# Optimization experiments

Measured on AMD Instinct MI355X. Metric: run time of the kernel, lower is better.

Reference implementation:

```python
import jax, jax.numpy as jnp
import numpy as np

N = 50000      # nodes
E = 600000     # edges (avg degree 12)
C = 128        # in/out channels
NF = 256       # SchNet num_filters (hardcoded in module)
EC = 64        # edge_channels (RBF expansion)


def ssp(x):
    # shifted softplus used by SchNet
    return jax.nn.softplus(x) - jnp.log(2.0).astype(x.dtype)


def setup_inputs() -> dict:
    key = jax.random.key(0)
    ks = jax.random.split(key, 16)
    def w(k, shape, fan_in):
        return jax.random.normal(k, shape, jnp.float32) * (1.0 / np.sqrt(fan_in))
    return {
        "x": jax.random.normal(ks[0], (N, C), jnp.float32),
        "edge_index": jax.random.randint(ks[1], (2, E), 0, N, jnp.int32),
        "edge_attr": jax.random.normal(ks[2], (E, EC), jnp.float32),
        "x_pos": jax.random.normal(ks[3], (N, 3), jnp.float32),
        # SchNet filter network: Linear(EC,NF) -> ssp -> Linear(NF,NF)
        "W_f1": w(ks[4], (EC, NF), EC), "b_f1": jnp.zeros((NF,), jnp.float32),
        "W_f2": w(ks[5], (NF, NF), NF), "b_f2": jnp.zeros((NF,), jnp.float32),
        # CFConv lin1 (no bias), lin2, then output lin3
        "W_lin1": w(ks[6], (C, NF), C),
        "W_lin2": w(ks[7], (NF, C), NF), "b_lin2": jnp.zeros((C,), jnp.float32),
        "W_lin3": w(ks[8], (C, C), C), "b_lin3": jnp.zeros((C,), jnp.float32),
        # edge MLP: Linear(EC + C, C) -> Tanh
        "W_e": w(ks[9], (EC + C, C), EC + C), "b_e": jnp.zeros((C,), jnp.float32),
    }


def reference(x, edge_index, edge_attr, x_pos,
              W_f1, b_f1, W_f2, b_f2,
              W_lin1, W_lin2, b_lin2, W_lin3, b_lin3,
              W_e, b_e):
    n = x.shape[0]
    row, col = edge_index[0], edge_index[1]

    # SchNet interaction (cfconv): edge filter net on edge_attr
    Wf = ssp(edge_attr @ W_f1 + b_f1) @ W_f2 + b_f2      # [E, NF]
    h = x @ W_lin1                                        # [N, NF]
    msg = h[col] * Wf                                     # [E, NF] gather + modulate
    agg = jax.ops.segment_sum(msg, row, num_segments=n)   # [N, NF] scatter-sum
    y = ssp(agg @ W_lin2 + b_lin2) @ W_lin3 + b_lin3      # [N, C]

    # relu + residual skip
    x_out = jax.nn.relu(y) + x

    # edge gather-MLP with residual on edge_attr
    e_in = jnp.concatenate([edge_attr, x_out[row] + x_out[col]], axis=-1)  # [E, EC+C]
    e_out = jnp.tanh(e_in @ W_e + b_e) + edge_attr if False else jnp.tanh(e_in @ W_e + b_e)
    # note: original adds residual only on edge_attr channels; shapes differ (C vs EC)
    # Linear maps to in_channels=C... but residual is `+ edge_attr` [E,EC]. In the repo
    # edge_channels == in_channels is required for this add; here EC != C, so we
    # follow the module math with EC projected: use the faithful form below.
    return x_out, e_out
```

## Files before the change

### kernel.cpp

```cpp
#include <hip/hip_runtime.h>

#define NN  50000
#define NE  600000
#define CC  128
#define NFF 256
#define ECH 64
#define EIN 192

typedef __attribute__((ext_vector_type(8))) short bf16x8;
typedef __attribute__((ext_vector_type(4))) short bf16x4;
typedef __attribute__((ext_vector_type(4))) float f32x4;
typedef __attribute__((ext_vector_type(4))) unsigned u32x4;
typedef __attribute__((ext_vector_type(2))) unsigned u32x2;

__device__ __forceinline__ float sspf(float v) {
    float e = __expf(-fabsf(v));
    return fmaxf(v, 0.f) + __logf(1.f + e) - 0.693147180559945f;
}
__device__ __forceinline__ float ftanh(float v) {
    float e = __expf(-2.f * fabsf(v));
    float r = (1.f - e) / (1.f + e);
    return copysignf(r, v);
}
__device__ __forceinline__ short bf16r(float f) {
    unsigned u = __float_as_uint(f);
    u = (u + 0x7FFFu + ((u >> 16) & 1u)) >> 16;
    return (short)u;
}
__device__ __forceinline__ unsigned cvtpk(float lo, float hi) {
    unsigned r;
    asm("v_cvt_pk_bf16_f32 %0, %1, %2" : "=v"(r) : "v"(lo), "v"(hi));
    return r;
}
__device__ __forceinline__ float bfu_lo(unsigned u) { return __uint_as_float(u << 16); }
__device__ __forceinline__ float bfu_hi(unsigned u) { return __uint_as_float(u & 0xffff0000u); }

#define PO_WF1 0
#define PO_WF2 16384
#define PO_WE  81920
#define PO_WL1 106496
#define PO_WL2 139264
#define PO_WL3 172032
#define P_TOT  188416
__global__ void kpack(const float* __restrict__ Wf1, const float* __restrict__ Wf2,
                      const float* __restrict__ We,  const float* __restrict__ Wl1,
                      const float* __restrict__ Wl2, const float* __restrict__ Wl3,
                      short* __restrict__ p) {
    int i = blockIdx.x * 256 + threadIdx.x;
    if (i < PO_WF2) {
        int t = i - PO_WF1;
        int j = t & 7, lane = (t >> 3) & 63, n16 = (t >> 9) & 15, ks = t >> 13;
        p[i] = bf16r(Wf1[(ks * 32 + (lane >> 4) * 8 + j) * NFF + n16 * 16 + (lane & 15)]);
    } else if (i < PO_WE) {
        int t = i - PO_WF2;
        int j = t & 7, lane = (t >> 3) & 63, n16 = (t >> 9) & 15, ks = t >> 13;
        int kp = ks * 32 + (lane >> 4) * 8 + j;
        int k = (kp >> 6) * 64 + (kp & 3) * 16 + ((kp >> 2) & 15);
        p[i] = bf16r(Wf2[k * NFF + n16 * 16 + (lane & 15)]);
    } else if (i < PO_WL1) {
        int t = i - PO_WE;
        int j = t & 7, lane = (t >> 3) & 63, n16 = (t >> 9) & 7, ks = t >> 12;
        p[i] = bf16r(We[(ks * 32 + (lane >> 4) * 8 + j) * CC + n16 * 16 + (lane & 15)]);
    } else if (i < PO_WL2) {
        int t = i - PO_WL1;
        int j = t & 7, lane = (t >> 3) & 63, n16 = (t >> 9) & 15, ks = t >> 13;
        p[i] = bf16r(Wl1[(ks * 32 + (lane >> 4) * 8 + j) * NFF + n16 * 16 + (lane & 15)]);
    } else if (i < PO_WL3) {
        int t = i - PO_WL2;
        int j = t & 7, lane = (t >> 3) & 63, n16 = (t >> 9) & 7, ks = t >> 12;
        int kp = ks * 32 + (lane >> 4) * 8 + j;
        int k = (kp >> 6) * 64 + (kp & 3) * 16 + ((kp >> 2) & 15);
        p[i] = bf16r(Wl2[k * CC + n16 * 16 + (lane & 15)]);
    } else if (i < P_TOT) {
        int t = i - PO_WL3;
        int j = t & 7, lane = (t >> 3) & 63, n16 = (t >> 9) & 7, ks = t >> 12;
        int kp = ks * 32 + (lane >> 4) * 8 + j;
        int k = (kp >> 5) * 32 + (kp & 1) * 16 + ((kp & 31) >> 1);
        p[i] = bf16r(Wl3[k * CC + n16 * 16 + (lane & 15)]);
    }
}

__global__ void k0_zero(float* __restrict__ p, long n4) {
    long i = (long)blockIdx.x * blockDim.x + threadIdx.x;
    long stride = (long)gridDim.x * blockDim.x;
    float4 z = {0.f, 0.f, 0.f, 0.f};
    for (; i < n4; i += stride) ((float4*)p)[i] = z;
}

__global__ void k_cnt(const int* __restrict__ eidx, int* __restrict__ cnt) {
    int e = blockIdx.x * 256 + threadIdx.x;
    if (e < NE) atomicAdd(&cnt[eidx[e]], 1);
}

__global__ __launch_bounds__(256) void k_scan1(const int* __restrict__ cnt,
                                               int* __restrict__ offw,
                                               int* __restrict__ bsum) {
    __shared__ int sw_[4];
    int i = blockIdx.x * 256 + threadIdx.x;
    int lane = threadIdx.x & 63, wv = threadIdx.x >> 6;
    int v = (i < NN) ? cnt[i] : 0;
    int inc = v;
    #pragma unroll
    for (int d = 1; d < 64; d <<= 1) {
        int t = __shfl_up(inc, d, 64);
        if (lane >= d) inc += t;
    }
    if (lane == 63) sw_[wv] = inc;
    __syncthreads();
    int woff = 0;
    #pragma unroll
    for (int k = 0; k < 4; ++k) woff += (k < wv) ? sw_[k] : 0;
    if (i < NN) offw[i] = woff + inc - v;
    if (threadIdx.x == 255) bsum[blockIdx.x] = woff + inc;
}

__global__ __launch_bounds__(256) void k_scan2(int* __restrict__ bsum, int nb) {
    __shared__ int sw_[4];
    int t = threadIdx.x;
    int lane = t & 63, wv = t >> 6;
    int v = (t < nb) ? bsum[t] : 0;
    int inc = v;
    #pragma unroll
    for (int d = 1; d < 64; d <<= 1) {
        int s = __shfl_up(inc, d, 64);
        if (lane >= d) inc += s;
    }
    if (lane == 63) sw_[wv] = inc;
    __syncthreads();
    int woff = 0;
    #pragma unroll
    for (int k = 0; k < 4; ++k) woff += (k < wv) ? sw_[k] : 0;
    if (t < nb) bsum[t] = woff + inc - v;
}

__global__ void k_scan3(int* __restrict__ offw, const int* __restrict__ bsum,
                        int* __restrict__ rowptr) {
    int i = blockIdx.x * 256 + threadIdx.x;
    if (i < NN) {
        int v = offw[i] + bsum[blockIdx.x];
        offw[i] = v;
        rowptr[i] = v;
    }
    if (i == 0) rowptr[NN] = NE;
}

__global__ void k_scatter(const int* __restrict__ eidx, int* __restrict__ offw,
                          int* __restrict__ dest) {
    int e = blockIdx.x * 256 + threadIdx.x;
    if (e < NE) dest[e] = atomicAdd(&offw[eidx[e]], 1);
}

__global__ __launch_bounds__(256) void k1_h(const float* __restrict__ x,
                                            const short* __restrict__ pW,
                                            short* __restrict__ h) {
    __shared__ char xS[32 * 256];
    int n0 = blockIdx.x * 32;
    int tid = threadIdx.x;
    int lane = tid & 63, w = tid >> 6, q = lane >> 4, l15 = lane & 15;
    {
        int r = tid >> 3, seg = tid & 7;
        int rr = min(n0 + r, NN - 1);
        const float4* src = (const float4*)(x + (size_t)rr * CC + seg * 16);
        float4 f0 = src[0], f1 = src[1], f2 = src[2], f3 = src[3];
        u32x4 c0 = {cvtpk(f0.x, f0.y), cvtpk(f0.z, f0.w), cvtpk(f1.x, f1.y), cvtpk(f1.z, f1.w)};
        u32x4 c1 = {cvtpk(f2.x, f2.y), cvtpk(f2.z, f2.w), cvtpk(f3.x, f3.y), cvtpk(f3.z, f3.w)};
        int sw = (r & 7) << 4;
        *(u32x4*)(xS + r * 256 + ((seg * 32) ^ sw)) = c0;
        *(u32x4*)(xS + r * 256 + ((seg * 32 + 16) ^ sw)) = c1;
    }
    __syncthreads();

    f32x4 acc[2][4];
    #pragma unroll
    for (int mf = 0; mf < 2; ++mf)
        #pragma unroll
        for (int nf = 0; nf < 4; ++nf) acc[mf][nf] = f32x4{0.f, 0.f, 0.f, 0.f};

    #pragma unroll
    for (int ks = 0; ks < 4; ++ks) {
        bf16x8 a[2];
        #pragma unroll
        for (int mf = 0; mf < 2; ++mf) {
            int row = mf * 16 + l15;
            a[mf] = *(const bf16x8*)(xS + row * 256 + ((ks * 64 + q * 16) ^ ((row & 7) << 4)));
        }
        #pragma unroll
        for (int nf = 0; nf < 4; ++nf) {
            bf16x8 b = *(const bf16x8*)(pW + PO_WL1 + (((ks * 16 + w * 4 + nf) * 64) + lane) * 8);
            #pragma unroll
            for (int mf = 0; mf < 2; ++mf)
                acc[mf][nf] = __builtin_amdgcn_mfma_f32_16x16x32_bf16(a[mf], b, acc[mf][nf], 0, 0, 0);
        }
    }
    #pragma unroll
    for (int mf = 0; mf < 2; ++mf) {
        #pragma unroll
        for (int r = 0; r < 4; ++r) {
            int n = n0 + mf * 16 + q * 4 + r;
            if (n < NN) {
                u32x2 v = {cvtpk(acc[mf][0][r], acc[mf][1][r]),
                           cvtpk(acc[mf][2][r], acc[mf][3][r])};
                *(u32x2*)(h + (size_t)n * NFF + w * 64 + l15 * 4) = v;
            }
        }
    }
}

__global__ __launch_bounds__(256, 4) void k2a_msg(
        const float* __restrict__ ea, const int* __restrict__ eidx,
        const int* __restrict__ dest,
        const short* __restrict__ pW, const float* __restrict__ bf1v,
        const float* __restrict__ bf2v,
        const short* __restrict__ h, short* __restrict__ msg) {
    __shared__ char t1S[64 * 512];
    __shared__ int colS[64], destS[64];
    char* eaS = t1S;
    int e0 = blockIdx.x * 64;
    int tid = threadIdx.x;
    int lane = tid & 63, w = tid >> 6;
    int q = lane >> 4, l15 = lane & 15;

    if (tid < 64) {
        colS[tid] = eidx[NE + e0 + tid];
        destS[tid] = dest[e0 + tid];
    }

    {
        int r = tid >> 2, cp = tid & 3;
        const float4* src = (const float4*)(ea + (size_t)(e0 + r) * ECH + cp * 16);
        float4 f0 = src[0], f1 = src[1], f2 = src[2], f3 = src[3];
        u32x4 c0 = {cvtpk(f0.x, f0.y), cvtpk(f0.z, f0.w), cvtpk(f1.x, f1.y), cvtpk(f1.z, f1.w)};
        u32x4 c1 = {cvtpk(f2.x, f2.y), cvtpk(f2.z, f2.w), cvtpk(f3.x, f3.y), cvtpk(f3.z, f3.w)};
        int sw = (r & 7) << 4;
        *(u32x4*)(eaS + r * 128 + ((cp * 32) ^ sw)) = c0;
        *(u32x4*)(eaS + r * 128 + ((cp * 32 + 16) ^ sw)) = c1;
    }
    __syncthreads();

    f32x4 acc[4][4];
    #pragma unroll
    for (int mf = 0; mf < 4; ++mf)
        #pragma unroll
        for (int nf = 0; nf < 4; ++nf) acc[mf][nf] = f32x4{0.f, 0.f, 0.f, 0.f};

    #pragma unroll
    for (int ks = 0; ks < 2; ++ks) {
        bf16x8 a[4];
        #pragma unroll
        for (int mf = 0; mf < 4; ++mf) {
            int row = mf * 16 + l15;
            a[mf] = *(const bf16x8*)(eaS + row * 128 + ((ks * 64 + q * 16) ^ ((row & 7) << 4)));
        }
        #pragma unroll
        for (int nf = 0; nf < 4; ++nf) {
            bf16x8 b = *(const bf16x8*)(pW + PO_WF1 + (((ks * 16 + w * 4 + nf) * 64) + lane) * 8);
            #pragma unroll
            for (int mf = 0; mf < 4; ++mf)
                acc[mf][nf] = __builtin_amdgcn_mfma_f32_16x16x32_bf16(a[mf], b, acc[mf][nf], 0, 0, 0);
        }
    }
    __syncthreads();

    {
        float bia[4];
        #pragma unroll
        for (int nf = 0; nf < 4; ++nf) bia[nf] = bf1v[w * 64 + nf * 16 + l15];
        #pragma unroll
        for (int mf = 0; mf < 4; ++mf) {
            #pragma unroll
            for (int r = 0; r < 4; ++r) {
                int row = mf * 16 + q * 4 + r;
                u32x2 v = {cvtpk(sspf(acc[mf][0][r] + bia[0]), sspf(acc[mf][1][r] + bia[1])),
                           cvtpk(sspf(acc[mf][2][r] + bia[2]), sspf(acc[mf][3][r] + bia[3]))};
                *(u32x2*)(t1S + row * 512 + ((w * 128 + l15 * 8) ^ ((row & 7) << 4))) = v;
            }
        }
    }
    __syncthreads();

    #pragma unroll
    for (int mf = 0; mf < 4; ++mf)
        #pragma unroll
        for (int nf = 0; nf < 4; ++nf) acc[mf][nf] = f32x4{0.f, 0.f, 0.f, 0.f};

    for (int ks = 0; ks < 8; ++ks) {
        bf16x8 a[4];
        #pragma unroll
        for (int mf = 0; mf < 4; ++mf) {
            int row = mf * 16 + l15;
            a[mf] = *(const bf16x8*)(t1S + row * 512 + ((ks * 64 + q * 16) ^ ((row & 7) << 4)));
        }
        #pragma unroll
        for (int nf = 0; nf < 4; ++nf) {
            bf16x8 b = *(const bf16x8*)(pW + PO_WF2 + (((ks * 16 + w * 4 + nf) * 64) + lane) * 8);
            #pragma unroll
            for (int mf = 0; mf < 4; ++mf)
                acc[mf][nf] = __builtin_amdgcn_mfma_f32_16x16x32_bf16(a[mf], b, acc[mf][nf], 0, 0, 0);
        }
    }
    __syncthreads();

    {
        int r = tid >> 2, ch = tid & 3;
        const short* hp = h + (size_t)colS[r] * NFF;
        int sw = (r & 7) << 4;
        #pragma unroll
        for (int i = 0; i < 8; ++i) {
            int chunk = ch + i * 4;
            bf16x8 v = *(const bf16x8*)(hp + chunk * 8);
            *(bf16x8*)(t1S + r * 512 + ((chunk * 16) ^ sw)) = v;
        }
    }
    __syncthreads();

    {
        float bia[4];
        #pragma unroll
        for (int nf = 0; nf < 4; ++nf) bia[nf] = bf2v[w * 64 + nf * 16 + l15];
        #pragma unroll
        for (int mf = 0; mf < 4; ++mf) {
            #pragma unroll
            for (int r = 0; r < 4; ++r) {
                int eloc = mf * 16 + q * 4 + r;
                u32x2 hv = *(const u32x2*)(t1S + eloc * 512 + ((w * 128 + l15 * 8) ^ ((eloc & 7) << 4)));
                float m0 = bfu_lo(hv[0]) * (acc[mf][0][r] + bia[0]);
                float m1 = bfu_hi(hv[0]) * (acc[mf][1][r] + bia[1]);
                float m2 = bfu_lo(hv[1]) * (acc[mf][2][r] + bia[2]);
                float m3 = bfu_hi(hv[1]) * (acc[mf][3][r] + bia[3]);
                u32x2 out = {cvtpk(m0, m1), cvtpk(m2, m3)};
                *(u32x2*)(msg + (size_t)destS[eloc] * NFF + w * 64 + l15 * 4) = out;
            }
        }
    }
}

__global__ __launch_bounds__(256) void k3_node(
        const short* __restrict__ msg, const int* __restrict__ rowptr,
        const short* __restrict__ pW, const float* __restrict__ bl2,
        const float* __restrict__ bl3,
        const float* __restrict__ x, float* __restrict__ xo) {
    __shared__ char aggS[32 * 512];
    __shared__ char t2S[32 * 256];
    int n0 = blockIdx.x * 32;
    int tid = threadIdx.x;
    int lane = tid & 63, w = tid >> 6, q = lane >> 4, l15 = lane & 15;

    {
        int nd = tid >> 3, c0 = (tid & 7) * 32;
        int n = n0 + nd;
        int p0 = 0, p1 = 0;
        if (n < NN) { p0 = rowptr[n]; p1 = rowptr[n + 1]; }
        float a[32];
        #pragma unroll
        for (int i = 0; i < 32; ++i) a[i] = 0.f;
        for (int p = p0; p < p1; ++p) {
            const short* mrow = msg + (size_t)p * NFF + c0;
            #pragma unroll
            for (int j = 0; j < 4; ++j) {
                u32x4 v = *(const u32x4*)(mrow + j * 8);
                #pragma unroll
                for (int k = 0; k < 4; ++k) {
                    a[j * 8 + 2 * k]     += bfu_lo(v[k]);
                    a[j * 8 + 2 * k + 1] += bfu_hi(v[k]);
                }
            }
        }
        int sw = (nd & 7) << 4;
        #pragma unroll
        for (int j = 0; j < 4; ++j) {
            u32x4 v = {cvtpk(a[j * 8 + 0], a[j * 8 + 1]), cvtpk(a[j * 8 + 2], a[j * 8 + 3]),
                       cvtpk(a[j * 8 + 4], a[j * 8 + 5]), cvtpk(a[j * 8 + 6], a[j * 8 + 7])};
            *(u32x4*)(aggS + nd * 512 + (((c0 + j * 8) * 2) ^ sw)) = v;
        }
    }
    __syncthreads();

    f32x4 acc[2][2];
    #pragma unroll
    for (int mf = 0; mf < 2; ++mf)
        #pragma unroll
        for (int nf = 0; nf < 2; ++nf) acc[mf][nf] = f32x4{0.f, 0.f, 0.f, 0.f};
    for (int ks = 0; ks < 8; ++ks) {
        bf16x8 a[2];
        #pragma unroll
        for (int mf = 0; mf < 2; ++mf) {
            int row = mf * 16 + l15;
            a[mf] = *(const bf16x8*)(aggS + row * 512 + ((ks * 64 + q * 16) ^ ((row & 7) << 4)));
        }
        #pragma unroll
        for (int nf = 0; nf < 2; ++nf) {
            bf16x8 b = *(const bf16x8*)(pW + PO_WL2 + (((ks * 8 + w * 2 + nf) * 64) + lane) * 8);
            #pragma unroll
            for (int mf = 0; mf < 2; ++mf)
                acc[mf][nf] = __builtin_amdgcn_mfma_f32_16x16x32_bf16(a[mf], b, acc[mf][nf], 0, 0, 0);
        }
    }
    {
        float bia[2];
        #pragma unroll
        for (int nf = 0; nf < 2; ++nf) bia[nf] = bl2[w * 32 + nf * 16 + l15];
        #pragma unroll
        for (int mf = 0; mf < 2; ++mf) {
            #pragma unroll
            for (int r = 0; r < 4; ++r) {
                int row = mf * 16 + q * 4 + r;
                unsigned u = cvtpk(sspf(acc[mf][0][r] + bia[0]), sspf(acc[mf][1][r] + bia[1]));
                *(unsigned*)(t2S + row * 256 + ((w * 64 + l15 * 4) ^ ((row & 7) << 4))) = u;
            }
        }
    }
    __syncthreads();

    f32x4 acc2[2][2];
    #pragma unroll
    for (int mf = 0; mf < 2; ++mf)
        #pragma unroll
        for (int nf = 0; nf < 2; ++nf) acc2[mf][nf] = f32x4{0.f, 0.f, 0.f, 0.f};
    #pragma unroll
    for (int ks = 0; ks < 4; ++ks) {
        bf16x8 a[2];
        #pragma unroll
        for (int mf = 0; mf < 2; ++mf) {
            int row = mf * 16 + l15;
            a[mf] = *(const bf16x8*)(t2S + row * 256 + ((ks * 64 + q * 16) ^ ((row & 7) << 4)));
        }
        #pragma unroll
        for (int nf = 0; nf < 2; ++nf) {
            bf16x8 b = *(const bf16x8*)(pW + PO_WL3 + (((ks * 8 + w * 2 + nf) * 64) + lane) * 8);
            #pragma unroll
            for (int mf = 0; mf < 2; ++mf)
                acc2[mf][nf] = __builtin_amdgcn_mfma_f32_16x16x32_bf16(a[mf], b, acc2[mf][nf], 0, 0, 0);
        }
    }
    #pragma unroll
    for (int nf = 0; nf < 2; ++nf) {
        int col = w * 32 + nf * 16 + l15;
        float bias = bl3[col];
        #pragma unroll
        for (int mf = 0; mf < 2; ++mf) {
            #pragma unroll
            for (int r = 0; r < 4; ++r) {
                int n = n0 + mf * 16 + q * 4 + r;
                if (n < NN) {
                    size_t o = (size_t)n * CC + col;
                    xo[o] = fmaxf(acc2[mf][nf][r] + bias, 0.f) + x[o];
                }
            }
        }
    }
}

__global__ __launch_bounds__(256) void k4_mfma(
        const float* __restrict__ ea, const int* __restrict__ eidx,
        const float* __restrict__ xo, const short* __restrict__ pW,
        const float* __restrict__ bev, float* __restrict__ eo) {
    __shared__ char aS[64 * 384];
    int e0 = blockIdx.x * 64;
    int tid = threadIdx.x;
    int lane = tid & 63, w = tid >> 6;
    int q = lane >> 4, l15 = lane & 15;

    {
        int r = tid >> 2, cp = tid & 3;
        const float4* src = (const float4*)(ea + (size_t)(e0 + r) * ECH + cp * 16);
        float4 f0 = src[0], f1 = src[1], f2 = src[2], f3 = src[3];
        u32x4 c0 = {cvtpk(f0.x, f0.y), cvtpk(f0.z, f0.w), cvtpk(f1.x, f1.y), cvtpk(f1.z, f1.w)};
        u32x4 c1 = {cvtpk(f2.x, f2.y), cvtpk(f2.z, f2.w), cvtpk(f3.x, f3.y), cvtpk(f3.z, f3.w)};
        int sw = (r & 7) << 4;
        *(u32x4*)(aS + r * 384 + ((cp * 32) ^ sw)) = c0;
        *(u32x4*)(aS + r * 384 + ((cp * 32 + 16) ^ sw)) = c1;
    }
    {
        int e = tid >> 2, p = tid & 3;
        int rr = eidx[e0 + e], cc = eidx[NE + e0 + e];
        const float4* xr = (const float4*)(xo + (size_t)rr * CC);
        const float4* xc = (const float4*)(xo + (size_t)cc * CC);
        int sw = (e & 7) << 4;
        #pragma unroll
        for (int it = 0; it < 8; ++it) {
            int fi = p + it * 4;
            float4 va = xr[fi], vb = xc[fi];
            u32x2 hv = {cvtpk(va.x + vb.x, va.y + vb.y), cvtpk(va.z + vb.z, va.w + vb.w)};
            int byte = (ECH + fi * 4) * 2;
            *(u32x2*)(aS + e * 384 + (byte ^ sw)) = hv;
        }
    }
    __syncthreads();

    f32x4 acc[8];
    #pragma unroll
    for (int nf = 0; nf < 8; ++nf) acc[nf] = f32x4{0.f, 0.f, 0.f, 0.f};

    #pragma unroll
    for (int ks = 0; ks < 6; ++ks) {
        int row = w * 16 + l15;
        bf16x8 a = *(const bf16x8*)(aS + row * 384 + ((ks * 64 + q * 16) ^ ((row & 7) << 4)));
        #pragma unroll
        for (int nf = 0; nf < 8; ++nf) {
            bf16x8 b = *(const bf16x8*)(pW + PO_WE + (((ks * 8 + nf) * 64) + lane) * 8);
            acc[nf] = __builtin_amdgcn_mfma_f32_16x16x32_bf16(a, b, acc[nf], 0, 0, 0);
        }
    }
    #pragma unroll
    for (int nf = 0; nf < 8; ++nf) {
        int col = nf * 16 + l15;
        float bias = bev[col];
        #pragma unroll
        for (int r = 0; r < 4; ++r) {
            int e = e0 + w * 16 + q * 4 + r;
            eo[(size_t)e * CC + col] = ftanh(acc[nf][r] + bias);
        }
    }
}

extern "C" void kernel_launch(void* const* d_in, const int* in_sizes, int n_in,
                              void* d_out, int out_size, void* d_ws, size_t ws_size,
                              hipStream_t stream) {
    const float* x   = (const float*)d_in[0];
    const int*   ei  = (const int*)d_in[1];
    const float* ea  = (const float*)d_in[2];
    const float* Wf1 = (const float*)d_in[4];
    const float* bf1 = (const float*)d_in[5];
    const float* Wf2 = (const float*)d_in[6];
    const float* bf2 = (const float*)d_in[7];
    const float* Wl1 = (const float*)d_in[8];
    const float* Wl2 = (const float*)d_in[9];
    const float* bl2 = (const float*)d_in[10];
    const float* Wl3 = (const float*)d_in[11];
    const float* bl3 = (const float*)d_in[12];
    const float* We  = (const float*)d_in[13];
    const float* be  = (const float*)d_in[14];

    float* xo = (float*)d_out;
    float* eo = xo + (size_t)NN * CC;

    short* h   = (short*)xo;
    short* msg = (short*)eo;

    short* pW    = (short*)d_ws;
    int* dest    = (int*)((char*)d_ws + 393216);
    int* cnt     = dest + NE;
    int* offw    = cnt + NN;
    int* rowptr  = offw + NN;
    int* bsum    = rowptr + NN + 1;

    const int NB = (NN + 255) / 256;

    kpack<<<P_TOT / 256, 256, 0, stream>>>(Wf1, Wf2, We, Wl1, Wl2, Wl3, pW);
    k0_zero<<<49, 256, 0, stream>>>((float*)cnt, NN / 4);
    k_cnt<<<(NE + 255) / 256, 256, 0, stream>>>(ei, cnt);
    k_scan1<<<NB, 256, 0, stream>>>(cnt, offw, bsum);
    k_scan2<<<1, 256, 0, stream>>>(bsum, NB);
    k_scan3<<<NB, 256, 0, stream>>>(offw, bsum, rowptr);
    k_scatter<<<(NE + 255) / 256, 256, 0, stream>>>(ei, offw, dest);
    k1_h<<<(NN + 31) / 32, 256, 0, stream>>>(x, pW, h);
    k2a_msg<<<NE / 64, 256, 0, stream>>>(ea, ei, dest, pW, bf1, bf2, h, msg);
    k3_node<<<(NN + 31) / 32, 256, 0, stream>>>(msg, rowptr, pW, bl2, bl3, x, xo);
    k4_mfma<<<NE / 64, 256, 0, stream>>>(ea, ei, xo, pW, be, eo);
}
```

Measured before the change: 548.1 us.

## Presort edges by row and fuse segment-sum into message kernel

```diff
diff --git a/kernel.cpp b/kernel.cpp
--- a/kernel.cpp
+++ b/kernel.cpp
@@ -144,10 +144,25 @@
     if (i == 0) rowptr[NN] = NE;
 }
 
-__global__ void k_scatter(const int* __restrict__ eidx, int* __restrict__ offw,
-                          int* __restrict__ dest) {
+__global__ void k_scatter(const int* __restrict__ eidx, const float* __restrict__ ea,
+                          int* __restrict__ offw, short* __restrict__ ea_s,
+                          int* __restrict__ col_s, int* __restrict__ row_s) {
     int e = blockIdx.x * 256 + threadIdx.x;
-    if (e < NE) dest[e] = atomicAdd(&offw[eidx[e]], 1);
+    if (e >= NE) return;
+    int r = eidx[e], c = eidx[NE + e];
+    int pos = atomicAdd(&offw[r], 1);
+    col_s[pos] = c;
+    row_s[pos] = r;
+    const float4* src = (const float4*)(ea + (size_t)e * ECH);
+    short* dst = ea_s + (size_t)pos * ECH;
+    #pragma unroll
+    for (int i = 0; i < 4; ++i) {
+        float4 f0 = src[4 * i], f1 = src[4 * i + 1], f2 = src[4 * i + 2], f3 = src[4 * i + 3];
+        u32x4 v0 = {cvtpk(f0.x, f0.y), cvtpk(f0.z, f0.w), cvtpk(f1.x, f1.y), cvtpk(f1.z, f1.w)};
+        u32x4 v1 = {cvtpk(f2.x, f2.y), cvtpk(f2.z, f2.w), cvtpk(f3.x, f3.y), cvtpk(f3.z, f3.w)};
+        *(u32x4*)(dst + i * 16) = v0;
+        *(u32x4*)(dst + i * 16 + 8) = v1;
+    }
 }
 
 __global__ __launch_bounds__(256) void k1_h(const float* __restrict__ x,
@@ -206,36 +221,23 @@
     }
 }
 
-__global__ __launch_bounds__(256, 4) void k2a_msg(
-        const float* __restrict__ ea, const int* __restrict__ eidx,
-        const int* __restrict__ dest,
+__global__ __launch_bounds__(256, 4) void k2b_agg(
+        const short* __restrict__ ea_s, const int* __restrict__ col_s,
+        const int* __restrict__ row_s,
         const short* __restrict__ pW, const float* __restrict__ bf1v,
         const float* __restrict__ bf2v,
-        const short* __restrict__ h, short* __restrict__ msg) {
+        const short* __restrict__ h, float* __restrict__ agg) {
     __shared__ char t1S[64 * 512];
-    __shared__ int colS[64], destS[64];
-    char* eaS = t1S;
-    int e0 = blockIdx.x * 64;
+    __shared__ int colS[64], rowS[64];
+    int s0 = blockIdx.x * 64;
     int tid = threadIdx.x;
     int lane = tid & 63, w = tid >> 6;
     int q = lane >> 4, l15 = lane & 15;
 
     if (tid < 64) {
-        colS[tid] = eidx[NE + e0 + tid];
-        destS[tid] = dest[e0 + tid];
-    }
-
-    {
-        int r = tid >> 2, cp = tid & 3;
-        const float4* src = (const float4*)(ea + (size_t)(e0 + r) * ECH + cp * 16);
-        float4 f0 = src[0], f1 = src[1], f2 = src[2], f3 = src[3];
-        u32x4 c0 = {cvtpk(f0.x, f0.y), cvtpk(f0.z, f0.w), cvtpk(f1.x, f1.y), cvtpk(f1.z, f1.w)};
-        u32x4 c1 = {cvtpk(f2.x, f2.y), cvtpk(f2.z, f2.w), cvtpk(f3.x, f3.y), cvtpk(f3.z, f3.w)};
-        int sw = (r & 7) << 4;
-        *(u32x4*)(eaS + r * 128 + ((cp * 32) ^ sw)) = c0;
-        *(u32x4*)(eaS + r * 128 + ((cp * 32 + 16) ^ sw)) = c1;
-    }
-    __syncthreads();
+        colS[tid] = col_s[s0 + tid];
+        rowS[tid] = row_s[s0 + tid];
+    }
 
     f32x4 acc[4][4];
     #pragma unroll
@@ -247,10 +249,8 @@
     for (int ks = 0; ks < 2; ++ks) {
         bf16x8 a[4];
         #pragma unroll
-        for (int mf = 0; mf < 4; ++mf) {
-            int row = mf * 16 + l15;
-            a[mf] = *(const bf16x8*)(eaS + row * 128 + ((ks * 64 + q * 16) ^ ((row & 7) << 4)));
-        }
+        for (int mf = 0; mf < 4; ++mf)
+            a[mf] = *(const bf16x8*)(ea_s + (size_t)(s0 + mf * 16 + l15) * ECH + ks * 32 + q * 8);
         #pragma unroll
         for (int nf = 0; nf < 4; ++nf) {
             bf16x8 b = *(const bf16x8*)(pW + PO_WF1 + (((ks * 16 + w * 4 + nf) * 64) + lane) * 8);
@@ -259,8 +259,6 @@
                 acc[mf][nf] = __builtin_amdgcn_mfma_f32_16x16x32_bf16(a[mf], b, acc[mf][nf], 0, 0, 0);
         }
     }
-    __syncthreads();
-
     {
         float bia[4];
         #pragma unroll
@@ -322,20 +320,48 @@
             #pragma unroll
             for (int r = 0; r < 4; ++r) {
                 int eloc = mf * 16 + q * 4 + r;
-                u32x2 hv = *(const u32x2*)(t1S + eloc * 512 + ((w * 128 + l15 * 8) ^ ((eloc & 7) << 4)));
+                char* addr = t1S + eloc * 512 + ((w * 128 + l15 * 8) ^ ((eloc & 7) << 4));
+                u32x2 hv = *(const u32x2*)addr;
                 float m0 = bfu_lo(hv[0]) * (acc[mf][0][r] + bia[0]);
                 float m1 = bfu_hi(hv[0]) * (acc[mf][1][r] + bia[1]);
                 float m2 = bfu_lo(hv[1]) * (acc[mf][2][r] + bia[2]);
                 float m3 = bfu_hi(hv[1]) * (acc[mf][3][r] + bia[3]);
                 u32x2 out = {cvtpk(m0, m1), cvtpk(m2, m3)};
-                *(u32x2*)(msg + (size_t)destS[eloc] * NFF + w * 64 + l15 * 4) = out;
-            }
-        }
+                *(u32x2*)addr = out;
+            }
+        }
+    }
+    __syncthreads();
+
+    if (tid < 128) {
+        int cp = tid;
+        float a0 = 0.f, a1 = 0.f;
+        int cur = rowS[0];
+        int astart = 0;
+        for (int e = 0; e < 64; ++e) {
+            int rw = rowS[e];
+            if (rw != cur) {
+                float* dst = agg + (size_t)cur * NFF + cp * 2;
+                if (astart > 0) {
+                    dst[0] = a0; dst[1] = a1;
+                } else {
+                    atomicAdd(dst, a0); atomicAdd(dst + 1, a1);
+                }
+                a0 = 0.f; a1 = 0.f;
+                cur = rw;
+                astart = e;
+            }
+            unsigned v = *(const unsigned*)(t1S + e * 512 + ((cp * 4) ^ ((e & 7) << 4)));
+            a0 += bfu_lo(v);
+            a1 += bfu_hi(v);
+        }
+        float* dst = agg + (size_t)cur * NFF + cp * 2;
+        atomicAdd(dst, a0); atomicAdd(dst + 1, a1);
     }
 }
 
 __global__ __launch_bounds__(256) void k3_node(
-        const short* __restrict__ msg, const int* __restrict__ rowptr,
+        const float* __restrict__ agg,
         const short* __restrict__ pW, const float* __restrict__ bl2,
         const float* __restrict__ bl3,
         const float* __restrict__ x, float* __restrict__ xo) {
@@ -348,22 +374,17 @@
     {
         int nd = tid >> 3, c0 = (tid & 7) * 32;
         int n = n0 + nd;
-        int p0 = 0, p1 = 0;
-        if (n < NN) { p0 = rowptr[n]; p1 = rowptr[n + 1]; }
         float a[32];
-        #pragma unroll
-        for (int i = 0; i < 32; ++i) a[i] = 0.f;
-        for (int p = p0; p < p1; ++p) {
-            const short* mrow = msg + (size_t)p * NFF + c0;
-            #pragma unroll
-            for (int j = 0; j < 4; ++j) {
-                u32x4 v = *(const u32x4*)(mrow + j * 8);
-                #pragma unroll
-                for (int k = 0; k < 4; ++k) {
-                    a[j * 8 + 2 * k]     += bfu_lo(v[k]);
-                    a[j * 8 + 2 * k + 1] += bfu_hi(v[k]);
-                }
-            }
+        if (n < NN) {
+            const float4* src = (const float4*)(agg + (size_t)n * NFF + c0);
+            #pragma unroll
+            for (int j = 0; j < 8; ++j) {
+                float4 v = src[j];
+                a[4 * j] = v.x; a[4 * j + 1] = v.y; a[4 * j + 2] = v.z; a[4 * j + 3] = v.w;
+            }
+        } else {
+            #pragma unroll
+            for (int i = 0; i < 32; ++i) a[i] = 0.f;
         }
         int sw = (nd & 7) << 4;
         #pragma unroll
@@ -534,12 +555,15 @@
     float* xo = (float*)d_out;
     float* eo = xo + (size_t)NN * CC;
 
-    short* h   = (short*)xo;
-    short* msg = (short*)eo;
+    short* h    = (short*)xo;
+    char*  top  = (char*)d_out + (size_t)out_size * sizeof(float);
+    short* ea_s = (short*)(top - (size_t)NE * ECH * 2);
+    int*   col_s = (int*)((char*)ea_s - (size_t)NE * 4);
+    int*   row_s = (int*)((char*)col_s - (size_t)NE * 4);
+    float* agg  = (float*)((char*)row_s - (size_t)NN * NFF * 4);
 
     short* pW    = (short*)d_ws;
-    int* dest    = (int*)((char*)d_ws + 393216);
-    int* cnt     = dest + NE;
+    int* cnt     = (int*)((char*)d_ws + 393216);
     int* offw    = cnt + NN;
     int* rowptr  = offw + NN;
     int* bsum    = rowptr + NN + 1;
@@ -547,14 +571,15 @@
     const int NB = (NN + 255) / 256;
 
     kpack<<<P_TOT / 256, 256, 0, stream>>>(Wf1, Wf2, We, Wl1, Wl2, Wl3, pW);
+    k0_zero<<<1024, 256, 0, stream>>>(agg, (long)NN * NFF / 4);
     k0_zero<<<49, 256, 0, stream>>>((float*)cnt, NN / 4);
     k_cnt<<<(NE + 255) / 256, 256, 0, stream>>>(ei, cnt);
     k_scan1<<<NB, 256, 0, stream>>>(cnt, offw, bsum);
     k_scan2<<<1, 256, 0, stream>>>(bsum, NB);
     k_scan3<<<NB, 256, 0, stream>>>(offw, bsum, rowptr);
-    k_scatter<<<(NE + 255) / 256, 256, 0, stream>>>(ei, offw, dest);
+    k_scatter<<<(NE + 255) / 256, 256, 0, stream>>>(ei, ea, offw, ea_s, col_s, row_s);
     k1_h<<<(NN + 31) / 32, 256, 0, stream>>>(x, pW, h);
-    k2a_msg<<<NE / 64, 256, 0, stream>>>(ea, ei, dest, pW, bf1, bf2, h, msg);
-    k3_node<<<(NN + 31) / 32, 256, 0, stream>>>(msg, rowptr, pW, bl2, bl3, x, xo);
+    k2b_agg<<<NE / 64, 256, 0, stream>>>(ea_s, col_s, row_s, pW, bf1, bf2, h, agg);
+    k3_node<<<(NN + 31) / 32, 256, 0, stream>>>(agg, pW, bl2, bl3, x, xo);
     k4_mfma<<<NE / 64, 256, 0, stream>>>(ea, ei, xo, pW, be, eo);
 }
```

Result: no change. 542.5 us (-1.0%).
